# Kernel optimization log

Measured on AMD Instinct MI355X. Metric: run time of the kernel, lower is better.

The kernel has to match this reference:

```python
import jax, jax.numpy as jnp
import numpy as np

B, L, M, IS = 64, 20, 16, 1024  # batch, headers/example, tokens/header, feature dim
EPS = 1e-12


def setup_inputs() -> dict:
    key = jax.random.key(0)
    ks = jax.random.split(key, 10)
    total = B * L
    s = 1.0 / np.sqrt(IS)
    return {
        "ctx": jax.random.normal(ks[0], (B, IS), jnp.float32),
        "wemb_hpu": jax.random.normal(ks[1], (total, M, IS), jnp.float32),
        "l_hpu": jnp.full((total,), M, jnp.int32),
        "l_hs": jnp.full((B,), L, jnp.int32),
        "U_w": jax.random.uniform(ks[2], (IS, IS), jnp.float32, -s, s),
        "U_b": jnp.zeros((IS,), jnp.float32),
        "V_w": jax.random.uniform(ks[3], (IS, IS), jnp.float32, -s, s),
        "V_b": jnp.zeros((IS,), jnp.float32),
        "enc_w": jax.random.uniform(ks[4], (IS, 2 * IS), jnp.float32, -s, s),
        "enc_b": jnp.zeros((IS,), jnp.float32),
        "gamma": jnp.ones((IS,), jnp.float32),
        "beta": jnp.zeros((IS,), jnp.float32),
    }


def reference(ctx, wemb_hpu, l_hpu, l_hs, U_w, U_b, V_w, V_b, enc_w, enc_b, gamma, beta):
    total = wemb_hpu.shape[0]
    bS = ctx.shape[0]
    seg = jnp.repeat(jnp.arange(bS), total // bS)  # header-unit -> example id (constant l_hs)
    wenc_u = ctx @ U_w.T + U_b                      # [B, IS]
    wenc_v = wemb_hpu @ V_w.T + V_b                 # [T, M, IS]
    # per-header attention over its M tokens: sum over feature dim, softmax over tokens
    attn = jnp.einsum('ti,tmi->tm', wenc_u[seg], wenc_v)   # [T, M]
    p = jax.nn.softmax(attn, axis=1)
    pooled = jnp.einsum('tm,tmi->ti', p, wemb_hpu)          # [T, IS]
    cat = jnp.concatenate([pooled, ctx[seg]], axis=-1)      # [T, 2*IS]
    h = cat @ enc_w.T + enc_b                               # [T, IS]
    # scatter into padded [B, mL_hs, IS] (constant lengths -> exact reshape)
    wenc_hs = h.reshape(bS, total // bS, -1)
    # TF-style LayerNorm (eps inside sqrt)
    u = wenc_hs.mean(-1, keepdims=True)
    s2 = ((wenc_hs - u) ** 2).mean(-1, keepdims=True)
    x = (wenc_hs - u) / jnp.sqrt(s2 + EPS)
    return gamma * x + beta
```

## Files before the change

### kernel.cpp

```cpp
#include <hip/hip_runtime.h>
#include <math.h>

#define TPB 256

constexpr int ISZ = 1024;
constexpr int NB  = 64;
constexpr int NL  = 20;
constexpr int NM  = 16;
constexpr int NT  = NB * NL;

typedef __attribute__((ext_vector_type(8))) short  bf16x8;
typedef __attribute__((ext_vector_type(4))) float  f32x4;

__device__ __forceinline__ unsigned short f2bf(float x) {
    unsigned int u = __builtin_bit_cast(unsigned int, x);
    unsigned int r = (u + 0x7fff + ((u >> 16) & 1)) >> 16;
    return (unsigned short)r;
}
__device__ __forceinline__ float bf2f(unsigned short h) {
    unsigned int u = ((unsigned int)h) << 16;
    return __builtin_bit_cast(float, u);
}
__device__ __forceinline__ void split4(float4 v, ushort4& h, ushort4& l) {
    h.x = f2bf(v.x); l.x = f2bf(v.x - bf2f(h.x));
    h.y = f2bf(v.y); l.y = f2bf(v.y - bf2f(h.y));
    h.z = f2bf(v.z); l.z = f2bf(v.z - bf2f(h.z));
    h.w = f2bf(v.w); l.w = f2bf(v.w - bf2f(h.w));
}

__device__ __forceinline__ void gld_lds16(const void* g, void* l) {
    __builtin_amdgcn_global_load_lds(
        (const __attribute__((address_space(1))) unsigned int*)g,
        (__attribute__((address_space(3))) unsigned int*)l, 16, 0, 0);
}

__global__ __launch_bounds__(TPB)
void prep(const float* __restrict__ ctx, const float* __restrict__ U_w,
          const float* __restrict__ V_w, const float* __restrict__ enc_w,
          const float* __restrict__ enc_b,
          unsigned short* __restrict__ ctxh, unsigned short* __restrict__ ctxl,
          unsigned short* __restrict__ Uwh,  unsigned short* __restrict__ Uwl,
          unsigned short* __restrict__ Vth,  unsigned short* __restrict__ Vtl,
          unsigned short* __restrict__ encb, unsigned short* __restrict__ encb2,
          float* __restrict__ cenc, float* __restrict__ uv)
{
    __shared__ float t[64][65];
    const int bx = blockIdx.x, tid = threadIdx.x;
    if (bx < 64) {
        int d = bx * 1024 + tid * 4;
        float4 v = *(const float4*)&ctx[d];
        ushort4 h, l; split4(v, h, l);
        *(ushort4*)&ctxh[d] = h; *(ushort4*)&ctxl[d] = l;
    } else if (bx < 1088) {
        int d = (bx - 64) * 1024 + tid * 4;
        float4 v = *(const float4*)&U_w[d];
        ushort4 h, l; split4(v, h, l);
        *(ushort4*)&Uwh[d] = h; *(ushort4*)&Uwl[d] = l;
    } else if (bx < 2112) {
        int d = (bx - 1088) * 1024 + tid * 4;
        float4 v = *(const float4*)&enc_w[(size_t)(d >> 10) * 2048 + (d & 1023)];
        ushort4 o = { f2bf(v.x), f2bf(v.y), f2bf(v.z), f2bf(v.w) };
        *(ushort4*)&encb[d] = o;
    } else if (bx < 3136) {
        int d = (bx - 2112) * 1024 + tid * 4;
        float4 v = *(const float4*)&enc_w[(size_t)(d >> 10) * 2048 + 1024 + (d & 1023)];
        ushort4 o = { f2bf(v.x), f2bf(v.y), f2bf(v.z), f2bf(v.w) };
        *(ushort4*)&encb2[d] = o;
    } else if (bx < 3392) {
        const int id = bx - 3136;
        const int r0 = (id >> 4) * 64, c0 = (id & 15) * 64;
        const int tr = tid >> 4, tc = (tid & 15) * 4;
        #pragma unroll
        for (int i = 0; i < 4; ++i) {
            float4 v = *(const float4*)&V_w[(size_t)(r0 + tr + 16 * i) * 1024 + c0 + tc];
            t[tr + 16 * i][tc + 0] = v.x; t[tr + 16 * i][tc + 1] = v.y;
            t[tr + 16 * i][tc + 2] = v.z; t[tr + 16 * i][tc + 3] = v.w;
        }
        __syncthreads();
        #pragma unroll
        for (int i = 0; i < 4; ++i) {
            int rr = tr + 16 * i;
            float4 v = { t[tc + 0][rr], t[tc + 1][rr], t[tc + 2][rr], t[tc + 3][rr] };
            ushort4 h, l; split4(v, h, l);
            *(ushort4*)&Vth[(size_t)(c0 + rr) * 1024 + r0 + tc] = h;
            *(ushort4*)&Vtl[(size_t)(c0 + rr) * 1024 + r0 + tc] = l;
        }
    } else if (bx < 3456) {
        int d = (bx - 3392) * 1024 + tid * 4;
        float4 v = *(const float4*)&enc_b[d & 1023];
        *(float4*)&cenc[d] = v;
    } else {
        int d = (bx - 3456) * 1024 + tid * 4;
        float4 z = {0.0f, 0.0f, 0.0f, 0.0f};
        *(float4*)&uv[d] = z;
    }
}

__device__ __forceinline__ void mfma_tile64(
    const unsigned short* __restrict__ Ab, const unsigned short* __restrict__ Bb,
    int n0, int kbeg, int nsteps, unsigned char* lds, f32x4 acc[2][2], int tid)
{
    const int wid = tid >> 6, lane = tid & 63;
    const int ln = lane & 15, kb = lane >> 4;
    const int wr = wid >> 1, wc = wid & 1;
    const int srow = lane >> 3, sbyte = (lane & 7) << 4;
    const int swz = sbyte ^ (srow << 4);

    for (int kt = 0; kt < nsteps; ++kt) {
        const int kbyte = (kbeg + kt * 64) * 2;
        #pragma unroll
        for (int i = 0; i < 2; ++i) {
            int r = wid * 8 + i * 32 + srow;
            gld_lds16((const char*)Ab + (size_t)r * 2048 + kbyte + swz,
                      (void*)(lds + wid * 1024 + i * 4096));
            gld_lds16((const char*)Bb + (size_t)(n0 + r) * 2048 + kbyte + swz,
                      (void*)(lds + 8192 + wid * 1024 + i * 4096));
        }
        __syncthreads();
        #pragma unroll
        for (int ks = 0; ks < 2; ++ks) {
            const int cb = ks * 64 + kb * 16;
            bf16x8 a[2], b[2];
            #pragma unroll
            for (int m = 0; m < 2; ++m) {
                int ra = wr * 32 + m * 16 + ln;
                a[m] = *(const bf16x8*)(lds + ra * 128 + (cb ^ ((ra & 7) << 4)));
            }
            #pragma unroll
            for (int n = 0; n < 2; ++n) {
                int rb = wc * 32 + n * 16 + ln;
                b[n] = *(const bf16x8*)(lds + 8192 + rb * 128 + (cb ^ ((rb & 7) << 4)));
            }
            #pragma unroll
            for (int m = 0; m < 2; ++m)
                #pragma unroll
                for (int n = 0; n < 2; ++n)
                    acc[m][n] = __builtin_amdgcn_mfma_f32_16x16x32_bf16(a[m], b[n], acc[m][n], 0, 0, 0);
        }
        __syncthreads();
    }
}

__device__ __forceinline__ void mfma_tile64_hl(
    const unsigned short* __restrict__ Ah, const unsigned short* __restrict__ Al,
    const unsigned short* __restrict__ Bh, const unsigned short* __restrict__ Bl,
    int n0, int kbeg, int nsteps, unsigned char* lds, f32x4 acc[2][2], int tid)
{
    const int wid = tid >> 6, lane = tid & 63;
    const int ln = lane & 15, kb = lane >> 4;
    const int wr = wid >> 1, wc = wid & 1;
    const int srow = lane >> 3, sbyte = (lane & 7) << 4;
    const int swz = sbyte ^ (srow << 4);

    for (int kt = 0; kt < nsteps; ++kt) {
        const int kbyte = (kbeg + kt * 64) * 2;
        #pragma unroll
        for (int i = 0; i < 2; ++i) {
            int r = wid * 8 + i * 32 + srow;
            size_t ga = (size_t)r * 2048 + kbyte + swz;
            size_t gb = (size_t)(n0 + r) * 2048 + kbyte + swz;
            gld_lds16((const char*)Ah + ga, (void*)(lds +     0 + wid * 1024 + i * 4096));
            gld_lds16((const char*)Al + ga, (void*)(lds +  8192 + wid * 1024 + i * 4096));
            gld_lds16((const char*)Bh + gb, (void*)(lds + 16384 + wid * 1024 + i * 4096));
            gld_lds16((const char*)Bl + gb, (void*)(lds + 24576 + wid * 1024 + i * 4096));
        }
        __syncthreads();
        #pragma unroll
        for (int ks = 0; ks < 2; ++ks) {
            const int cb = ks * 64 + kb * 16;
            bf16x8 ah[2], al[2], bh[2], bl[2];
            #pragma unroll
            for (int m = 0; m < 2; ++m) {
                int ra = wr * 32 + m * 16 + ln;
                int off = ra * 128 + (cb ^ ((ra & 7) << 4));
                ah[m] = *(const bf16x8*)(lds + off);
                al[m] = *(const bf16x8*)(lds + 8192 + off);
            }
            #pragma unroll
            for (int n = 0; n < 2; ++n) {
                int rb = wc * 32 + n * 16 + ln;
                int off = rb * 128 + (cb ^ ((rb & 7) << 4));
                bh[n] = *(const bf16x8*)(lds + 16384 + off);
                bl[n] = *(const bf16x8*)(lds + 24576 + off);
            }
            #pragma unroll
            for (int m = 0; m < 2; ++m)
                #pragma unroll
                for (int n = 0; n < 2; ++n) {
                    acc[m][n] = __builtin_amdgcn_mfma_f32_16x16x32_bf16(ah[m], bh[n], acc[m][n], 0, 0, 0);
                    acc[m][n] = __builtin_amdgcn_mfma_f32_16x16x32_bf16(ah[m], bl[n], acc[m][n], 0, 0, 0);
                    acc[m][n] = __builtin_amdgcn_mfma_f32_16x16x32_bf16(al[m], bh[n], acc[m][n], 0, 0, 0);
                }
        }
        __syncthreads();
    }
}

__global__ __launch_bounds__(TPB)
void gemm_small(const unsigned short* __restrict__ ctxh,
                const unsigned short* __restrict__ ctxl,
                const unsigned short* __restrict__ Uwh,
                const unsigned short* __restrict__ Uwl,
                const unsigned short* __restrict__ encb2,
                const float* __restrict__ U_b,
                unsigned short* __restrict__ wenc_uh,
                unsigned short* __restrict__ wenc_ul,
                float* __restrict__ cenc)
{
    __shared__ __align__(16) unsigned char lds[32768];
    const int tid = threadIdx.x;
    const int n0 = blockIdx.x * 64;
    const int wid = tid >> 6, lane = tid & 63;
    const int wr = wid >> 1, wc = wid & 1;
    const int cl = lane & 15, rg = lane >> 4;

    f32x4 acc[2][2] = {};
    if (blockIdx.y == 8) {
        mfma_tile64_hl(ctxh, ctxl, Uwh, Uwl, n0, 0, 16, lds, acc, tid);
        #pragma unroll
        for (int m = 0; m < 2; ++m)
            #pragma unroll
            for (int n = 0; n < 2; ++n) {
                int col = n0 + wc * 32 + n * 16 + cl;
                #pragma unroll
                for (int j = 0; j < 4; ++j) {
                    int row = wr * 32 + m * 16 + rg * 4 + j;
                    float s = acc[m][n][j] + U_b[col];
                    unsigned short hi = f2bf(s);
                    wenc_uh[(size_t)row * ISZ + col] = hi;
                    wenc_ul[(size_t)row * ISZ + col] = f2bf(s - bf2f(hi));
                }
            }
    } else {
        mfma_tile64(ctxh, encb2, n0, blockIdx.y * 128, 2, lds, acc, tid);
        #pragma unroll
        for (int m = 0; m < 2; ++m)
            #pragma unroll
            for (int n = 0; n < 2; ++n) {
                int col = n0 + wc * 32 + n * 16 + cl;
                #pragma unroll
                for (int j = 0; j < 4; ++j) {
                    int row = wr * 32 + m * 16 + rg * 4 + j;
                    atomicAdd(&cenc[(size_t)row * ISZ + col], acc[m][n][j]);
                }
            }
    }
}

__global__ __launch_bounds__(TPB)
void gemm_uv(const unsigned short* __restrict__ wenc_uh,
             const unsigned short* __restrict__ wenc_ul,
             const unsigned short* __restrict__ Vth,
             const unsigned short* __restrict__ Vtl,
             float* __restrict__ uv)
{
    __shared__ __align__(16) unsigned char lds[32768];
    const int tid = threadIdx.x;
    const int n0 = blockIdx.x * 64;

    f32x4 acc[2][2] = {};
    mfma_tile64_hl(wenc_uh, wenc_ul, Vth, Vtl, n0, blockIdx.y * 128, 2, lds, acc, tid);

    const int wid = tid >> 6, lane = tid & 63;
    const int wr = wid >> 1, wc = wid & 1;
    const int cl = lane & 15, rg = lane >> 4;
    #pragma unroll
    for (int m = 0; m < 2; ++m)
        #pragma unroll
        for (int n = 0; n < 2; ++n) {
            int col = n0 + wc * 32 + n * 16 + cl;
            #pragma unroll
            for (int j = 0; j < 4; ++j) {
                int row = wr * 32 + m * 16 + rg * 4 + j;
                atomicAdd(&uv[(size_t)row * ISZ + col], acc[m][n][j]);
            }
        }
}

__global__ __launch_bounds__(TPB)
void attn_pool(const float* __restrict__ wemb, const float* __restrict__ uv,
               unsigned short* __restrict__ pooledb)
{
    const int t   = blockIdx.x;
    const int b   = t / NL;
    const int tid = threadIdx.x;
    const int lane = tid & 63, wid = tid >> 6;
    __shared__ float red[16][4];
    __shared__ float att[16];

    const float* w = wemb + (size_t)t * NM * ISZ;
    const int j0 = tid << 2;
    float4 u4 = *(const float4*)&uv[(size_t)b * ISZ + j0];

    float4 wv[NM];
    float part[NM];
    #pragma unroll
    for (int m = 0; m < NM; ++m) {
        wv[m] = *(const float4*)&w[m * ISZ + j0];
        part[m] = wv[m].x * u4.x + wv[m].y * u4.y + wv[m].z * u4.z + wv[m].w * u4.w;
    }
    #pragma unroll
    for (int m = 0; m < NM; ++m) {
        float v = part[m];
        #pragma unroll
        for (int off = 32; off > 0; off >>= 1) v += __shfl_down(v, off, 64);
        if (lane == 0) red[m][wid] = v;
    }
    __syncthreads();
    if (tid < NM) att[tid] = red[tid][0] + red[tid][1] + red[tid][2] + red[tid][3];
    __syncthreads();

    float mx = att[0];
    #pragma unroll
    for (int m = 1; m < NM; ++m) mx = fmaxf(mx, att[m]);
    float p[NM], s = 0.0f;
    #pragma unroll
    for (int m = 0; m < NM; ++m) { p[m] = __expf(att[m] - mx); s += p[m]; }
    float inv = 1.0f / s;

    float4 acc = {0.0f, 0.0f, 0.0f, 0.0f};
    #pragma unroll
    for (int m = 0; m < NM; ++m) {
        float pm = p[m] * inv;
        acc.x += pm * wv[m].x; acc.y += pm * wv[m].y;
        acc.z += pm * wv[m].z; acc.w += pm * wv[m].w;
    }
    ushort4 o;
    o.x = f2bf(acc.x); o.y = f2bf(acc.y); o.z = f2bf(acc.z); o.w = f2bf(acc.w);
    *(ushort4*)&pooledb[(size_t)t * ISZ + j0] = o;
}

__global__ __launch_bounds__(TPB)
void gemm_enc_mfma(const unsigned short* __restrict__ Abf,
                   const unsigned short* __restrict__ Bbf,
                   const float* __restrict__ cenc,
                   float* __restrict__ C)
{
    __shared__ __align__(16) unsigned char lds[24576];
    const int tid  = threadIdx.x;
    const int wid  = tid >> 6, lane = tid & 63;
    const int m0   = blockIdx.y * 128;
    const int n0   = blockIdx.x * 64;
    const int ln   = lane & 15, kb = lane >> 4;
    const int wr   = wid >> 1, wc = wid & 1;
    const int srow = lane >> 3, sbyte = (lane & 7) << 4;
    const int swz  = sbyte ^ (srow << 4);

    f32x4 acc[4][2] = {};
    const char* Abase = (const char*)Abf;
    const char* Bbase = (const char*)Bbf;

    for (int kt = 0; kt < 16; ++kt) {
        const int kbyte = kt * 128;
        #pragma unroll
        for (int i = 0; i < 4; ++i) {
            int r = wid * 8 + i * 32 + srow;
            gld_lds16(Abase + ((size_t)(m0 + r) * ISZ) * 2 + kbyte + swz,
                      (void*)(lds + wid * 1024 + i * 4096));
        }
        #pragma unroll
        for (int i = 0; i < 2; ++i) {
            int r = wid * 8 + i * 32 + srow;
            gld_lds16(Bbase + ((size_t)(n0 + r) * ISZ) * 2 + kbyte + swz,
                      (void*)(lds + 16384 + wid * 1024 + i * 4096));
        }
        __syncthreads();

        #pragma unroll
        for (int ks = 0; ks < 2; ++ks) {
            const int cb = (ks * 64 + kb * 16);
            bf16x8 a[4], b[2];
            #pragma unroll
            for (int m = 0; m < 4; ++m) {
                int ra = wr * 64 + m * 16 + ln;
                a[m] = *(const bf16x8*)(lds + ra * 128 + (cb ^ ((ra & 7) << 4)));
            }
            #pragma unroll
            for (int n = 0; n < 2; ++n) {
                int rb = wc * 32 + n * 16 + ln;
                b[n] = *(const bf16x8*)(lds + 16384 + rb * 128 + (cb ^ ((rb & 7) << 4)));
            }
            #pragma unroll
            for (int m = 0; m < 4; ++m)
                #pragma unroll
                for (int n = 0; n < 2; ++n)
                    acc[m][n] = __builtin_amdgcn_mfma_f32_16x16x32_bf16(a[m], b[n], acc[m][n], 0, 0, 0);
        }
        __syncthreads();
    }

    const int cl = lane & 15, rg = lane >> 4;
    #pragma unroll
    for (int m = 0; m < 4; ++m) {
        #pragma unroll
        for (int n = 0; n < 2; ++n) {
            int col = n0 + wc * 32 + n * 16 + cl;
            #pragma unroll
            for (int j = 0; j < 4; ++j) {
                int row = m0 + wr * 64 + m * 16 + rg * 4 + j;
                C[(size_t)row * ISZ + col] = acc[m][n][j] + cenc[(size_t)(row / NL) * ISZ + col];
            }
        }
    }
}

__global__ __launch_bounds__(TPB)
void layernorm_inplace(float* __restrict__ x, const float* __restrict__ gamma,
                       const float* __restrict__ beta)
{
    __shared__ float rs[4], rs2[4];
    __shared__ float mu_s, rstd_s;
    const int t = blockIdx.x;
    const int tid = threadIdx.x;
    const int lane = tid & 63, wid = tid >> 6;
    const int c = tid << 2;

    float4 v = *(const float4*)&x[(size_t)t * ISZ + c];
    float s  = v.x + v.y + v.z + v.w;
    float s2 = v.x * v.x + v.y * v.y + v.z * v.z + v.w * v.w;
    #pragma unroll
    for (int off = 32; off > 0; off >>= 1) {
        s  += __shfl_down(s, off, 64);
        s2 += __shfl_down(s2, off, 64);
    }
    if (lane == 0) { rs[wid] = s; rs2[wid] = s2; }
    __syncthreads();
    if (tid == 0) {
        float S  = rs[0] + rs[1] + rs[2] + rs[3];
        float S2 = rs2[0] + rs2[1] + rs2[2] + rs2[3];
        float m  = S / ISZ;
        float var = S2 / ISZ - m * m;
        mu_s  = m;
        rstd_s = rsqrtf(var + 1e-12f);
    }
    __syncthreads();
    const float mu = mu_s, rstd = rstd_s;
    float4 g  = *(const float4*)&gamma[c];
    float4 be = *(const float4*)&beta[c];
    float4 o;
    o.x = g.x * (v.x - mu) * rstd + be.x;
    o.y = g.y * (v.y - mu) * rstd + be.y;
    o.z = g.z * (v.z - mu) * rstd + be.z;
    o.w = g.w * (v.w - mu) * rstd + be.w;
    *(float4*)&x[(size_t)t * ISZ + c] = o;
}

extern "C" void kernel_launch(void* const* d_in, const int* in_sizes, int n_in,
                              void* d_out, int out_size, void* d_ws, size_t ws_size,
                              hipStream_t stream)
{
    const float* ctx   = (const float*)d_in[0];
    const float* wemb  = (const float*)d_in[1];
    const float* U_w   = (const float*)d_in[4];
    const float* U_b   = (const float*)d_in[5];
    const float* V_w   = (const float*)d_in[6];
    const float* enc_w = (const float*)d_in[8];
    const float* enc_b = (const float*)d_in[9];
    const float* gamma = (const float*)d_in[10];
    const float* beta  = (const float*)d_in[11];
    float* out = (float*)d_out;

    float* ws   = (float*)d_ws;
    float* uv   = ws;
    float* cenc = ws + NB * ISZ;
    unsigned short* p = (unsigned short*)(ws + 2 * NB * ISZ);
    unsigned short* ctxh    = p;  p += NB * ISZ;
    unsigned short* ctxl    = p;  p += NB * ISZ;
    unsigned short* wenc_uh = p;  p += NB * ISZ;
    unsigned short* wenc_ul = p;  p += NB * ISZ;
    unsigned short* Uwh     = p;  p += ISZ * ISZ;
    unsigned short* Uwl     = p;  p += ISZ * ISZ;
    unsigned short* Vth     = p;  p += ISZ * ISZ;
    unsigned short* Vtl     = p;  p += ISZ * ISZ;
    unsigned short* encb    = p;  p += ISZ * ISZ;
    unsigned short* encb2   = p;  p += ISZ * ISZ;
    unsigned short* pooledb = p;

    prep<<<3520, TPB, 0, stream>>>(ctx, U_w, V_w, enc_w, enc_b,
                                   ctxh, ctxl, Uwh, Uwl, Vth, Vtl,
                                   encb, encb2, cenc, uv);

    gemm_small<<<dim3(16, 9), TPB, 0, stream>>>(ctxh, ctxl, Uwh, Uwl, encb2,
                                                U_b, wenc_uh, wenc_ul, cenc);

    gemm_uv<<<dim3(16, 8), TPB, 0, stream>>>(wenc_uh, wenc_ul, Vth, Vtl, uv);

    attn_pool<<<NT, TPB, 0, stream>>>(wemb, uv, pooledb);

    gemm_enc_mfma<<<dim3(16, 10), TPB, 0, stream>>>(pooledb, encb, cenc, out);

    layernorm_inplace<<<NT, TPB, 0, stream>>>(out, gamma, beta);
}
```

Before: 67.62 us.

## Fuse bf16 splitting into GEMM staging and merge prep work into consumer kernels

Drops the monolithic prep kernel that wrote bf16 hi/lo copies of ctx, U_w and enc_w to global memory. Those conversions now happen in the GEMM staging loads, straight from fp32 into LDS. The small GEMMs (ctx@U_w with split-K atomics, ctx@enc_w second half) run in the same launch as the V_w transpose. The enc_w first-half conversion rides along with attn_pool. This cuts global traffic and removes a serialized launch, at the cost of register-path staging instead of async global_load_lds and a new init kernel for bias and zero setup.

```diff
diff --git a/kernel.cpp b/kernel.cpp
--- a/kernel.cpp
+++ b/kernel.cpp
@@ -27,52 +27,138 @@
     h.z = f2bf(v.z); l.z = f2bf(v.z - bf2f(h.z));
     h.w = f2bf(v.w); l.w = f2bf(v.w - bf2f(h.w));
 }
-
 __device__ __forceinline__ void gld_lds16(const void* g, void* l) {
     __builtin_amdgcn_global_load_lds(
         (const __attribute__((address_space(1))) unsigned int*)g,
         (__attribute__((address_space(3))) unsigned int*)l, 16, 0, 0);
 }
 
-__global__ __launch_bounds__(TPB)
-void prep(const float* __restrict__ ctx, const float* __restrict__ U_w,
-          const float* __restrict__ V_w, const float* __restrict__ enc_w,
-          const float* __restrict__ enc_b,
-          unsigned short* __restrict__ ctxh, unsigned short* __restrict__ ctxl,
-          unsigned short* __restrict__ Uwh,  unsigned short* __restrict__ Uwl,
-          unsigned short* __restrict__ Vth,  unsigned short* __restrict__ Vtl,
-          unsigned short* __restrict__ encb, unsigned short* __restrict__ encb2,
-          float* __restrict__ cenc, float* __restrict__ uv)
-{
-    __shared__ float t[64][65];
-    const int bx = blockIdx.x, tid = threadIdx.x;
-    if (bx < 64) {
-        int d = bx * 1024 + tid * 4;
-        float4 v = *(const float4*)&ctx[d];
+
+__device__ __forceinline__ void stage_hl(const float* __restrict__ src, int ld,
+                                         int kbeg, unsigned char* ldsH,
+                                         unsigned char* ldsL, int tid)
+{
+    #pragma unroll
+    for (int r = 0; r < 4; ++r) {
+        int idx = r * 256 + tid;
+        int row = idx >> 4, cg = (idx & 15) << 2;
+        float4 v = *(const float4*)&src[(size_t)row * ld + kbeg + cg];
         ushort4 h, l; split4(v, h, l);
-        *(ushort4*)&ctxh[d] = h; *(ushort4*)&ctxl[d] = l;
-    } else if (bx < 1088) {
-        int d = (bx - 64) * 1024 + tid * 4;
-        float4 v = *(const float4*)&U_w[d];
-        ushort4 h, l; split4(v, h, l);
-        *(ushort4*)&Uwh[d] = h; *(ushort4*)&Uwl[d] = l;
-    } else if (bx < 2112) {
-        int d = (bx - 1088) * 1024 + tid * 4;
-        float4 v = *(const float4*)&enc_w[(size_t)(d >> 10) * 2048 + (d & 1023)];
-        ushort4 o = { f2bf(v.x), f2bf(v.y), f2bf(v.z), f2bf(v.w) };
-        *(ushort4*)&encb[d] = o;
-    } else if (bx < 3136) {
-        int d = (bx - 2112) * 1024 + tid * 4;
-        float4 v = *(const float4*)&enc_w[(size_t)(d >> 10) * 2048 + 1024 + (d & 1023)];
-        ushort4 o = { f2bf(v.x), f2bf(v.y), f2bf(v.z), f2bf(v.w) };
-        *(ushort4*)&encb2[d] = o;
-    } else if (bx < 3392) {
-        const int id = bx - 3136;
+        int boff = row * 128 + ((cg << 1) ^ ((row & 7) << 4));
+        *(ushort4*)(ldsH + boff) = h;
+        *(ushort4*)(ldsL + boff) = l;
+    }
+}
+__device__ __forceinline__ void stage_h(const float* __restrict__ src, int ld,
+                                        int kbeg, unsigned char* ldsH, int tid)
+{
+    #pragma unroll
+    for (int r = 0; r < 4; ++r) {
+        int idx = r * 256 + tid;
+        int row = idx >> 4, cg = (idx & 15) << 2;
+        float4 v = *(const float4*)&src[(size_t)row * ld + kbeg + cg];
+        ushort4 h = { f2bf(v.x), f2bf(v.y), f2bf(v.z), f2bf(v.w) };
+        int boff = row * 128 + ((cg << 1) ^ ((row & 7) << 4));
+        *(ushort4*)(ldsH + boff) = h;
+    }
+}
+
+__device__ __forceinline__ void comp_hl(const unsigned char* lds, f32x4 acc[2][2], int tid)
+{
+    const int wid = tid >> 6, lane = tid & 63;
+    const int ln = lane & 15, kb = lane >> 4;
+    const int wr = wid >> 1, wc = wid & 1;
+    #pragma unroll
+    for (int ks = 0; ks < 2; ++ks) {
+        const int cb = ks * 64 + kb * 16;
+        bf16x8 ah[2], al[2], bh[2], bl[2];
+        #pragma unroll
+        for (int m = 0; m < 2; ++m) {
+            int ra = wr * 32 + m * 16 + ln;
+            int off = ra * 128 + (cb ^ ((ra & 7) << 4));
+            ah[m] = *(const bf16x8*)(lds + off);
+            al[m] = *(const bf16x8*)(lds + 8192 + off);
+        }
+        #pragma unroll
+        for (int n = 0; n < 2; ++n) {
+            int rb = wc * 32 + n * 16 + ln;
+            int off = rb * 128 + (cb ^ ((rb & 7) << 4));
+            bh[n] = *(const bf16x8*)(lds + 16384 + off);
+            bl[n] = *(const bf16x8*)(lds + 24576 + off);
+        }
+        #pragma unroll
+        for (int m = 0; m < 2; ++m)
+            #pragma unroll
+            for (int n = 0; n < 2; ++n) {
+                acc[m][n] = __builtin_amdgcn_mfma_f32_16x16x32_bf16(ah[m], bh[n], acc[m][n], 0, 0, 0);
+                acc[m][n] = __builtin_amdgcn_mfma_f32_16x16x32_bf16(ah[m], bl[n], acc[m][n], 0, 0, 0);
+                acc[m][n] = __builtin_amdgcn_mfma_f32_16x16x32_bf16(al[m], bh[n], acc[m][n], 0, 0, 0);
+            }
+    }
+}
+__device__ __forceinline__ void comp_h(const unsigned char* lds, f32x4 acc[2][2], int tid)
+{
+    const int wid = tid >> 6, lane = tid & 63;
+    const int ln = lane & 15, kb = lane >> 4;
+    const int wr = wid >> 1, wc = wid & 1;
+    #pragma unroll
+    for (int ks = 0; ks < 2; ++ks) {
+        const int cb = ks * 64 + kb * 16;
+        bf16x8 ah[2], bh[2];
+        #pragma unroll
+        for (int m = 0; m < 2; ++m) {
+            int ra = wr * 32 + m * 16 + ln;
+            ah[m] = *(const bf16x8*)(lds + ra * 128 + (cb ^ ((ra & 7) << 4)));
+        }
+        #pragma unroll
+        for (int n = 0; n < 2; ++n) {
+            int rb = wc * 32 + n * 16 + ln;
+            bh[n] = *(const bf16x8*)(lds + 16384 + rb * 128 + (cb ^ ((rb & 7) << 4)));
+        }
+        #pragma unroll
+        for (int m = 0; m < 2; ++m)
+            #pragma unroll
+            for (int n = 0; n < 2; ++n)
+                acc[m][n] = __builtin_amdgcn_mfma_f32_16x16x32_bf16(ah[m], bh[n], acc[m][n], 0, 0, 0);
+    }
+}
+
+__global__ __launch_bounds__(TPB)
+void init_small(float* __restrict__ wenc_u, float* __restrict__ cenc,
+                float* __restrict__ uv,
+                const float* __restrict__ U_b, const float* __restrict__ enc_b)
+{
+    int i = blockIdx.x * TPB + threadIdx.x;
+    int i4 = i << 2;
+    int col = i4 & (ISZ - 1);
+    if (i4 < NB * ISZ) {
+        *(float4*)&wenc_u[i4] = *(const float4*)&U_b[col];
+    } else if (i4 < 2 * NB * ISZ) {
+        *(float4*)&cenc[i4 - NB * ISZ] = *(const float4*)&enc_b[col];
+    } else {
+        float4 z = {0.f, 0.f, 0.f, 0.f};
+        *(float4*)&uv[i4 - 2 * NB * ISZ] = z;
+    }
+}
+
+__global__ __launch_bounds__(TPB)
+void small_and_vt(const float* __restrict__ ctx, const float* __restrict__ U_w,
+                  const float* __restrict__ enc_w, const float* __restrict__ V_w,
+                  float* __restrict__ wenc_u, float* __restrict__ cenc,
+                  unsigned short* __restrict__ Vth, unsigned short* __restrict__ Vtl)
+{
+    __shared__ __align__(16) unsigned char smem[32768];
+    const int tid = threadIdx.x;
+    const int bid = blockIdx.x;
+
+    if (bid >= 256) {
+        float (*t)[65] = (float(*)[65])smem;
+        const int id = bid - 256;
         const int r0 = (id >> 4) * 64, c0 = (id & 15) * 64;
         const int tr = tid >> 4, tc = (tid & 15) * 4;
         #pragma unroll
         for (int i = 0; i < 4; ++i) {
-            float4 v = *(const float4*)&V_w[(size_t)(r0 + tr + 16 * i) * 1024 + c0 + tc];
+            float4 v = *(const float4*)&V_w[(size_t)(r0 + tr + 16 * i) * ISZ + c0 + tc];
             t[tr + 16 * i][tc + 0] = v.x; t[tr + 16 * i][tc + 1] = v.y;
             t[tr + 16 * i][tc + 2] = v.z; t[tr + 16 * i][tc + 3] = v.w;
         }
@@ -82,186 +168,81 @@
             int rr = tr + 16 * i;
             float4 v = { t[tc + 0][rr], t[tc + 1][rr], t[tc + 2][rr], t[tc + 3][rr] };
             ushort4 h, l; split4(v, h, l);
-            *(ushort4*)&Vth[(size_t)(c0 + rr) * 1024 + r0 + tc] = h;
-            *(ushort4*)&Vtl[(size_t)(c0 + rr) * 1024 + r0 + tc] = l;
-        }
-    } else if (bx < 3456) {
-        int d = (bx - 3392) * 1024 + tid * 4;
-        float4 v = *(const float4*)&enc_b[d & 1023];
-        *(float4*)&cenc[d] = v;
-    } else {
-        int d = (bx - 3456) * 1024 + tid * 4;
-        float4 z = {0.0f, 0.0f, 0.0f, 0.0f};
-        *(float4*)&uv[d] = z;
-    }
-}
-
-__device__ __forceinline__ void mfma_tile64(
-    const unsigned short* __restrict__ Ab, const unsigned short* __restrict__ Bb,
-    int n0, int kbeg, int nsteps, unsigned char* lds, f32x4 acc[2][2], int tid)
-{
-    const int wid = tid >> 6, lane = tid & 63;
-    const int ln = lane & 15, kb = lane >> 4;
-    const int wr = wid >> 1, wc = wid & 1;
-    const int srow = lane >> 3, sbyte = (lane & 7) << 4;
-    const int swz = sbyte ^ (srow << 4);
-
-    for (int kt = 0; kt < nsteps; ++kt) {
-        const int kbyte = (kbeg + kt * 64) * 2;
-        #pragma unroll
-        for (int i = 0; i < 2; ++i) {
-            int r = wid * 8 + i * 32 + srow;
-            gld_lds16((const char*)Ab + (size_t)r * 2048 + kbyte + swz,
-                      (void*)(lds + wid * 1024 + i * 4096));
-            gld_lds16((const char*)Bb + (size_t)(n0 + r) * 2048 + kbyte + swz,
-                      (void*)(lds + 8192 + wid * 1024 + i * 4096));
-        }
-        __syncthreads();
-        #pragma unroll
-        for (int ks = 0; ks < 2; ++ks) {
-            const int cb = ks * 64 + kb * 16;
-            bf16x8 a[2], b[2];
-            #pragma unroll
-            for (int m = 0; m < 2; ++m) {
-                int ra = wr * 32 + m * 16 + ln;
-                a[m] = *(const bf16x8*)(lds + ra * 128 + (cb ^ ((ra & 7) << 4)));
-            }
-            #pragma unroll
-            for (int n = 0; n < 2; ++n) {
-                int rb = wc * 32 + n * 16 + ln;
-                b[n] = *(const bf16x8*)(lds + 8192 + rb * 128 + (cb ^ ((rb & 7) << 4)));
-            }
-            #pragma unroll
-            for (int m = 0; m < 2; ++m)
-                #pragma unroll
-                for (int n = 0; n < 2; ++n)
-                    acc[m][n] = __builtin_amdgcn_mfma_f32_16x16x32_bf16(a[m], b[n], acc[m][n], 0, 0, 0);
-        }
-        __syncthreads();
-    }
-}
-
-__device__ __forceinline__ void mfma_tile64_hl(
-    const unsigned short* __restrict__ Ah, const unsigned short* __restrict__ Al,
-    const unsigned short* __restrict__ Bh, const unsigned short* __restrict__ Bl,
-    int n0, int kbeg, int nsteps, unsigned char* lds, f32x4 acc[2][2], int tid)
-{
-    const int wid = tid >> 6, lane = tid & 63;
-    const int ln = lane & 15, kb = lane >> 4;
-    const int wr = wid >> 1, wc = wid & 1;
-    const int srow = lane >> 3, sbyte = (lane & 7) << 4;
-    const int swz = sbyte ^ (srow << 4);
-
-    for (int kt = 0; kt < nsteps; ++kt) {
-        const int kbyte = (kbeg + kt * 64) * 2;
-        #pragma unroll
-        for (int i = 0; i < 2; ++i) {
-            int r = wid * 8 + i * 32 + srow;
-            size_t ga = (size_t)r * 2048 + kbyte + swz;
-            size_t gb = (size_t)(n0 + r) * 2048 + kbyte + swz;
-            gld_lds16((const char*)Ah + ga, (void*)(lds +     0 + wid * 1024 + i * 4096));
-            gld_lds16((const char*)Al + ga, (void*)(lds +  8192 + wid * 1024 + i * 4096));
-            gld_lds16((const char*)Bh + gb, (void*)(lds + 16384 + wid * 1024 + i * 4096));
-            gld_lds16((const char*)Bl + gb, (void*)(lds + 24576 + wid * 1024 + i * 4096));
-        }
-        __syncthreads();
-        #pragma unroll
-        for (int ks = 0; ks < 2; ++ks) {
-            const int cb = ks * 64 + kb * 16;
-            bf16x8 ah[2], al[2], bh[2], bl[2];
-            #pragma unroll
-            for (int m = 0; m < 2; ++m) {
-                int ra = wr * 32 + m * 16 + ln;
-                int off = ra * 128 + (cb ^ ((ra & 7) << 4));
-                ah[m] = *(const bf16x8*)(lds + off);
-                al[m] = *(const bf16x8*)(lds + 8192 + off);
-            }
-            #pragma unroll
-            for (int n = 0; n < 2; ++n) {
-                int rb = wc * 32 + n * 16 + ln;
-                int off = rb * 128 + (cb ^ ((rb & 7) << 4));
-                bh[n] = *(const bf16x8*)(lds + 16384 + off);
-                bl[n] = *(const bf16x8*)(lds + 24576 + off);
-            }
-            #pragma unroll
-            for (int m = 0; m < 2; ++m)
-                #pragma unroll
-                for (int n = 0; n < 2; ++n) {
-                    acc[m][n] = __builtin_amdgcn_mfma_f32_16x16x32_bf16(ah[m], bh[n], acc[m][n], 0, 0, 0);
-                    acc[m][n] = __builtin_amdgcn_mfma_f32_16x16x32_bf16(ah[m], bl[n], acc[m][n], 0, 0, 0);
-                    acc[m][n] = __builtin_amdgcn_mfma_f32_16x16x32_bf16(al[m], bh[n], acc[m][n], 0, 0, 0);
-                }
-        }
-        __syncthreads();
-    }
-}
-
-__global__ __launch_bounds__(TPB)
-void gemm_small(const unsigned short* __restrict__ ctxh,
-                const unsigned short* __restrict__ ctxl,
-                const unsigned short* __restrict__ Uwh,
-                const unsigned short* __restrict__ Uwl,
-                const unsigned short* __restrict__ encb2,
-                const float* __restrict__ U_b,
-                unsigned short* __restrict__ wenc_uh,
-                unsigned short* __restrict__ wenc_ul,
-                float* __restrict__ cenc)
-{
-    __shared__ __align__(16) unsigned char lds[32768];
-    const int tid = threadIdx.x;
-    const int n0 = blockIdx.x * 64;
+            *(ushort4*)&Vth[(size_t)(c0 + rr) * ISZ + r0 + tc] = h;
+            *(ushort4*)&Vtl[(size_t)(c0 + rr) * ISZ + r0 + tc] = l;
+        }
+        return;
+    }
+
+    const int n0 = (bid & 15) * 64;
+    const int yv = bid >> 4;
+    const bool isU = (yv >= 8);
+    const int kbeg = (isU ? (yv - 8) : yv) * 128;
+
+    f32x4 acc[2][2] = {};
+    for (int kt = 0; kt < 2; ++kt) {
+        const int kk = kbeg + kt * 64;
+        if (isU) {
+            stage_hl(ctx, ISZ, kk, smem, smem + 8192, tid);
+            stage_hl(U_w + (size_t)n0 * ISZ, ISZ, kk, smem + 16384, smem + 24576, tid);
+        } else {
+            stage_h(ctx, ISZ, kk, smem, tid);
+            stage_h(enc_w + (size_t)n0 * 2048 + 1024, 2048, kk, smem + 16384, tid);
+        }
+        __syncthreads();
+        if (isU) comp_hl(smem, acc, tid);
+        else     comp_h(smem, acc, tid);
+        __syncthreads();
+    }
+
     const int wid = tid >> 6, lane = tid & 63;
     const int wr = wid >> 1, wc = wid & 1;
     const int cl = lane & 15, rg = lane >> 4;
-
-    f32x4 acc[2][2] = {};
-    if (blockIdx.y == 8) {
-        mfma_tile64_hl(ctxh, ctxl, Uwh, Uwl, n0, 0, 16, lds, acc, tid);
-        #pragma unroll
-        for (int m = 0; m < 2; ++m)
-            #pragma unroll
-            for (int n = 0; n < 2; ++n) {
-                int col = n0 + wc * 32 + n * 16 + cl;
-                #pragma unroll
-                for (int j = 0; j < 4; ++j) {
-                    int row = wr * 32 + m * 16 + rg * 4 + j;
-                    float s = acc[m][n][j] + U_b[col];
-                    unsigned short hi = f2bf(s);
-                    wenc_uh[(size_t)row * ISZ + col] = hi;
-                    wenc_ul[(size_t)row * ISZ + col] = f2bf(s - bf2f(hi));
-                }
-            }
-    } else {
-        mfma_tile64(ctxh, encb2, n0, blockIdx.y * 128, 2, lds, acc, tid);
-        #pragma unroll
-        for (int m = 0; m < 2; ++m)
-            #pragma unroll
-            for (int n = 0; n < 2; ++n) {
-                int col = n0 + wc * 32 + n * 16 + cl;
-                #pragma unroll
-                for (int j = 0; j < 4; ++j) {
-                    int row = wr * 32 + m * 16 + rg * 4 + j;
-                    atomicAdd(&cenc[(size_t)row * ISZ + col], acc[m][n][j]);
-                }
-            }
-    }
-}
-
-__global__ __launch_bounds__(TPB)
-void gemm_uv(const unsigned short* __restrict__ wenc_uh,
-             const unsigned short* __restrict__ wenc_ul,
+    float* dst = isU ? wenc_u : cenc;
+    #pragma unroll
+    for (int m = 0; m < 2; ++m)
+        #pragma unroll
+        for (int n = 0; n < 2; ++n) {
+            int col = n0 + wc * 32 + n * 16 + cl;
+            #pragma unroll
+            for (int j = 0; j < 4; ++j) {
+                int row = wr * 32 + m * 16 + rg * 4 + j;
+                atomicAdd(&dst[(size_t)row * ISZ + col], acc[m][n][j]);
+            }
+        }
+}
+
+__global__ __launch_bounds__(TPB)
+void gemm_uv(const float* __restrict__ wenc_u,
              const unsigned short* __restrict__ Vth,
              const unsigned short* __restrict__ Vtl,
              float* __restrict__ uv)
 {
-    __shared__ __align__(16) unsigned char lds[32768];
+    __shared__ __align__(16) unsigned char smem[32768];
     const int tid = threadIdx.x;
     const int n0 = blockIdx.x * 64;
+    const int kbeg = blockIdx.y * 128;
+    const int wid = tid >> 6, lane = tid & 63;
+    const int srow = lane >> 3, sbyte = (lane & 7) << 4;
+    const int swz = sbyte ^ (srow << 4);
 
     f32x4 acc[2][2] = {};
-    mfma_tile64_hl(wenc_uh, wenc_ul, Vth, Vtl, n0, blockIdx.y * 128, 2, lds, acc, tid);
-
-    const int wid = tid >> 6, lane = tid & 63;
+    for (int kt = 0; kt < 2; ++kt) {
+        const int kk = kbeg + kt * 64;
+        const int kbyte = kk * 2;
+        #pragma unroll
+        for (int i = 0; i < 2; ++i) {
+            int r = wid * 8 + i * 32 + srow;
+            size_t gb = (size_t)(n0 + r) * 2048 + kbyte + swz;
+            gld_lds16((const char*)Vth + gb, (void*)(smem + 16384 + wid * 1024 + i * 4096));
+            gld_lds16((const char*)Vtl + gb, (void*)(smem + 24576 + wid * 1024 + i * 4096));
+        }
+        stage_hl(wenc_u, ISZ, kk, smem, smem + 8192, tid);
+        __syncthreads();
+        comp_hl(smem, acc, tid);
+        __syncthreads();
+    }
+
     const int wr = wid >> 1, wc = wid & 1;
     const int cl = lane & 15, rg = lane >> 4;
     #pragma unroll
@@ -278,9 +259,18 @@
 }
 
 __global__ __launch_bounds__(TPB)
-void attn_pool(const float* __restrict__ wemb, const float* __restrict__ uv,
-               unsigned short* __restrict__ pooledb)
-{
+void attn_encconv(const float* __restrict__ wemb, const float* __restrict__ uv,
+                  unsigned short* __restrict__ pooledb,
+                  const float* __restrict__ enc_w, unsigned short* __restrict__ encb)
+{
+    if (blockIdx.x >= NT) {
+        const int row = blockIdx.x - NT;
+        const int c = threadIdx.x << 2;
+        float4 v = *(const float4*)&enc_w[(size_t)row * 2048 + c];
+        ushort4 o = { f2bf(v.x), f2bf(v.y), f2bf(v.z), f2bf(v.w) };
+        *(ushort4*)&encb[(size_t)row * ISZ + c] = o;
+        return;
+    }
     const int t   = blockIdx.x;
     const int b   = t / NL;
     const int tid = threadIdx.x;
@@ -460,32 +450,25 @@
     const float* beta  = (const float*)d_in[11];
     float* out = (float*)d_out;
 
-    float* ws   = (float*)d_ws;
-    float* uv   = ws;
-    float* cenc = ws + NB * ISZ;
-    unsigned short* p = (unsigned short*)(ws + 2 * NB * ISZ);
-    unsigned short* ctxh    = p;  p += NB * ISZ;
-    unsigned short* ctxl    = p;  p += NB * ISZ;
-    unsigned short* wenc_uh = p;  p += NB * ISZ;
-    unsigned short* wenc_ul = p;  p += NB * ISZ;
-    unsigned short* Uwh     = p;  p += ISZ * ISZ;
-    unsigned short* Uwl     = p;  p += ISZ * ISZ;
+    float* ws     = (float*)d_ws;
+    float* wenc_u = ws;
+    float* cenc   = ws + 1 * NB * ISZ;
+    float* uv     = ws + 2 * NB * ISZ;
+    unsigned short* p = (unsigned short*)(ws + 3 * NB * ISZ);
     unsigned short* Vth     = p;  p += ISZ * ISZ;
     unsigned short* Vtl     = p;  p += ISZ * ISZ;
     unsigned short* encb    = p;  p += ISZ * ISZ;
-    unsigned short* encb2   = p;  p += ISZ * ISZ;
     unsigned short* pooledb = p;
 
-    prep<<<3520, TPB, 0, stream>>>(ctx, U_w, V_w, enc_w, enc_b,
-                                   ctxh, ctxl, Uwh, Uwl, Vth, Vtl,
-                                   encb, encb2, cenc, uv);
-
-    gemm_small<<<dim3(16, 9), TPB, 0, stream>>>(ctxh, ctxl, Uwh, Uwl, encb2,
-                                                U_b, wenc_uh, wenc_ul, cenc);
-
-    gemm_uv<<<dim3(16, 8), TPB, 0, stream>>>(wenc_uh, wenc_ul, Vth, Vtl, uv);
-
-    attn_pool<<<NT, TPB, 0, stream>>>(wemb, uv, pooledb);
+    init_small<<<(3 * NB * ISZ / 4 + TPB - 1) / TPB, TPB, 0, stream>>>(
+        wenc_u, cenc, uv, U_b, enc_b);
+
+    small_and_vt<<<512, TPB, 0, stream>>>(ctx, U_w, enc_w, V_w,
+                                          wenc_u, cenc, Vth, Vtl);
+
+    gemm_uv<<<dim3(16, 8), TPB, 0, stream>>>(wenc_u, Vth, Vtl, uv);
+
+    attn_encconv<<<NT + ISZ, TPB, 0, stream>>>(wemb, uv, pooledb, enc_w, encb);
 
     gemm_enc_mfma<<<dim3(16, 10), TPB, 0, stream>>>(pooledb, encb, cenc, out);
 
```

After: 59.77 us. 1.13x faster.
